# Kernel tuning notes

Measured on AMD Instinct MI355X. Metric: run time of the kernel, lower is better.

## Reference

```python
import jax, jax.numpy as jnp
import numpy as np

# Static multi-scale pyramid (H, W per level); Nv = sum(H*W) = 13294
SPATIAL = np.array([[100, 100], [50, 50], [25, 25], [13, 13]], dtype=np.int64)
B, C, NH, NL, NP = 2, 256, 8, 4, 4
D = C // NH
TOT = NH * NL * NP


def setup_inputs() -> dict:
    key = jax.random.key(0)
    ks = jax.random.split(key, 10)
    Nv = int((SPATIAL[:, 0] * SPATIAL[:, 1]).sum())
    Nq = Nv
    query = jax.random.normal(ks[0], (B, Nq, C), dtype=jnp.float32)
    value = jax.random.normal(ks[1], (B, Nv, C), dtype=jnp.float32)
    reference_points = jax.random.uniform(ks[2], (B, Nq, NL, 2), minval=0.05, maxval=0.95, dtype=jnp.float32)
    spatial_shapes = jnp.asarray(SPATIAL)
    level_start_index = jnp.asarray(np.concatenate([[0], np.cumsum(SPATIAL[:, 0] * SPATIAL[:, 1])[:-1]]))
    # sampling_offsets: small random weight + the rotated-grid bias from _reset_parameters
    W_off = 0.01 * jax.random.normal(ks[3], (C, TOT * 2), dtype=jnp.float32)
    thetas = np.arange(NH, dtype=np.float64) * (2.0 * np.pi / NH)
    grid = np.stack([np.cos(thetas), np.sin(thetas)], -1)
    grid = grid / np.abs(grid).max(-1, keepdims=True)
    grid = np.tile(grid[:, None, None, :], (1, NL, NP, 1)) * (np.arange(NP) + 1)[None, None, :, None]
    b_off = jnp.asarray(grid.reshape(-1), dtype=jnp.float32)
    W_attn = 0.01 * jax.random.normal(ks[4], (C, TOT), dtype=jnp.float32)
    b_attn = jnp.zeros((TOT,), jnp.float32)
    W_val = jax.random.normal(ks[5], (C, C), dtype=jnp.float32) / np.sqrt(C)
    b_val = jnp.zeros((C,), jnp.float32)
    W_out = jax.random.normal(ks[6], (C, C), dtype=jnp.float32) / np.sqrt(C)
    b_out = jnp.zeros((C,), jnp.float32)
    return {"query": query, "value": value, "reference_points": reference_points,
            "spatial_shapes": spatial_shapes, "level_start_index": level_start_index,
            "W_off": W_off, "b_off": b_off, "W_attn": W_attn, "b_attn": b_attn,
            "W_val": W_val, "b_val": b_val, "W_out": W_out, "b_out": b_out}


def _bilinear(vl, loc, H, W):
    # vl: [B, h, H*W, D]; loc: [B, Nq, h, P, 2] normalized (x, y) in [0,1]
    # Matches F.grid_sample(mode='bilinear', padding_mode='zeros', align_corners=False)
    Bb, h, _, Dd = vl.shape
    Nq, P = loc.shape[1], loc.shape[3]
    x = loc[..., 0] * W - 0.5
    y = loc[..., 1] * H - 0.5
    x0 = jnp.floor(x)
    y0 = jnp.floor(y)
    fx = x - x0
    fy = y - y0
    out = jnp.zeros((Bb, h, Nq * P, Dd), vl.dtype)
    corners = ((0, 0, (1 - fx) * (1 - fy)), (1, 0, fx * (1 - fy)),
               (0, 1, (1 - fx) * fy), (1, 1, fx * fy))
    for dx, dy, w in corners:
        xi = x0 + dx
        yi = y0 + dy
        valid = (xi >= 0) & (xi < W) & (yi >= 0) & (yi < H)
        idx = (jnp.clip(yi, 0, H - 1) * W + jnp.clip(xi, 0, W - 1)).astype(jnp.int32)
        idx = idx.transpose(0, 2, 1, 3).reshape(Bb, h, Nq * P)          # [B,h,Nq*P]
        wv = (w * valid).transpose(0, 2, 1, 3).reshape(Bb, h, Nq * P)   # [B,h,Nq*P]
        g = jnp.take_along_axis(vl, idx[..., None], axis=2)             # [B,h,Nq*P,D]
        out = out + g * wv[..., None]
    return out.reshape(Bb, h, Nq, P, Dd)


def reference(query, value, reference_points, spatial_shapes, level_start_index,
              W_off, b_off, W_attn, b_attn, W_val, b_val, W_out, b_out):
    Bb, Nq, Cc = query.shape
    v = (value @ W_val + b_val).reshape(Bb, -1, NH, D)                  # [B,Nv,h,D]
    off = (query @ W_off + b_off).reshape(Bb, Nq, NH, NL, NP, 2)
    attn = jax.nn.softmax((query @ W_attn + b_attn).reshape(Bb, Nq, NH, NL * NP), axis=-1)
    attn = attn.reshape(Bb, Nq, NH, NL, NP)
    # offset normalizer is (W, H) per level
    norm = jnp.asarray(SPATIAL[:, ::-1].copy(), dtype=query.dtype)      # [L,2]
    loc = reference_points[:, :, None, :, None, :] + off / norm[None, None, None, :, None, :]
    starts = np.concatenate([[0], np.cumsum(SPATIAL[:, 0] * SPATIAL[:, 1])])
    out_acc = jnp.zeros((Bb, NH, Nq, D), query.dtype)
    for l in range(NL):
        H, W = int(SPATIAL[l, 0]), int(SPATIAL[l, 1])
        vl = v[:, int(starts[l]):int(starts[l + 1])].transpose(0, 2, 1, 3)  # [B,h,HW,D]
        samp = _bilinear(vl, loc[:, :, :, l], H, W)                     # [B,h,Nq,P,D]
        w_l = attn[:, :, :, l].transpose(0, 2, 1, 3)                    # [B,h,Nq,P]
        out_acc = out_acc + jnp.einsum('bhqpd,bhqp->bhqd', samp, w_l)
    out = out_acc.transpose(0, 2, 1, 3).reshape(Bb, Nq, Cc)
    return out @ W_out + b_out
```

## Files before the change

### kernel.cpp

```cpp
#include <hip/hip_runtime.h>
#include <hip/hip_bf16.h>

#define NQ  13294
#define NV  13294
#define BQ  26588

typedef __attribute__((ext_vector_type(8))) short short8;
typedef __attribute__((ext_vector_type(4))) float f32x4;

static __device__ __forceinline__ ushort f2bf(float f) {
    unsigned int x = __float_as_uint(f);
    unsigned int r = (x + 0x7fffu + ((x >> 16) & 1u)) >> 16;
    return (ushort)r;
}
static __device__ __forceinline__ uint cvtpk_bf16(float a, float b) {
    uint r;
    asm("v_cvt_pk_bf16_f32 %0, %1, %2" : "=v"(r) : "v"(a), "v"(b));
    return r;
}
static __device__ __forceinline__ uint cvtpk_f16(float a, float b) {
    uint r;
    asm("v_cvt_pkrtz_f16_f32 %0, %1, %2" : "=v"(r) : "v"(a), "v"(b));
    return r;
}
static __device__ __forceinline__ float f16lo(uint u) {
    _Float16 h; ushort t = (ushort)(u & 0xffffu);
    __builtin_memcpy(&h, &t, 2); return (float)h;
}
static __device__ __forceinline__ float f16hi(uint u) {
    _Float16 h; ushort t = (ushort)(u >> 16);
    __builtin_memcpy(&h, &t, 2); return (float)h;
}

__global__ __launch_bounds__(256) void prep_weights(
    const float* __restrict__ Wv, const float* __restrict__ Wo,
    const float* __restrict__ Wa, const float* __restrict__ Wu,
    const float* __restrict__ bo, const float* __restrict__ ba,
    ushort* __restrict__ tWv, ushort* __restrict__ tWoa,
    ushort* __restrict__ tWu, float* __restrict__ boa) {
    int i = blockIdx.x * 256 + threadIdx.x;
    if (i < 65536) {
        int n = i >> 8, k = i & 255;
        tWv[i] = f2bf(Wv[k * 256 + n]);
    } else if (i < 65536 + 98304) {
        int j = i - 65536;
        int n = j >> 8, k = j & 255;
        tWoa[j] = f2bf(n < 256 ? Wo[k * 256 + n] : Wa[k * 128 + (n - 256)]);
    } else if (i < 229376) {
        int j = i - 163840;
        int n = j >> 8, k = j & 255;
        tWu[j] = f2bf(Wu[k * 256 + n]);
    } else if (i < 229760) {
        int j = i - 229376;
        boa[j] = j < 256 ? bo[j] : ba[j - 256];
    }
}

#define LDP 40

template<int AF32>
static __device__ __forceinline__ void gemm_core(
    const void* __restrict__ Aptr, const ushort* __restrict__ Bt,
    const float* __restrict__ bias, void* __restrict__ Cout,
    int M, int N, int out_mode, int mblk, int nblk,
    ushort* sA, ushort* sB) {
    const int tid = threadIdx.x;
    const int wid = tid >> 6;
    const int lane = tid & 63;
    const int row0 = mblk * 128;
    const int col0 = nblk * 128;
    const int wr = (wid >> 1) * 64;
    const int wc = (wid & 1) * 64;

    f32x4 acc[4][4];
#pragma unroll
    for (int m = 0; m < 4; ++m)
#pragma unroll
        for (int n = 0; n < 4; ++n) acc[m][n] = (f32x4){0.f, 0.f, 0.f, 0.f};

    for (int kk = 0; kk < 256; kk += 32) {
        __syncthreads();
#pragma unroll
        for (int it = 0; it < 2; ++it) {
            int chunk = tid + it * 256;
            int r = chunk >> 2;
            int seg = chunk & 3;
            int gr = row0 + r; gr = gr < M ? gr : M - 1;
            uint4 wa;
            if (AF32) {
                const float* Af = (const float*)Aptr + (size_t)gr * 256 + kk + seg * 8;
                float4 f0 = *reinterpret_cast<const float4*>(Af);
                float4 f1 = *reinterpret_cast<const float4*>(Af + 4);
                wa.x = cvtpk_bf16(f0.x, f0.y);
                wa.y = cvtpk_bf16(f0.z, f0.w);
                wa.z = cvtpk_bf16(f1.x, f1.y);
                wa.w = cvtpk_bf16(f1.z, f1.w);
            } else {
                wa = *reinterpret_cast<const uint4*>((const ushort*)Aptr + (size_t)gr * 256 + kk + seg * 8);
            }
            *reinterpret_cast<uint4*>(&sA[r * LDP + seg * 8]) = wa;
            int gc = col0 + r;
            uint4 vb4 = *reinterpret_cast<const uint4*>(Bt + (size_t)gc * 256 + kk + seg * 8);
            *reinterpret_cast<uint4*>(&sB[r * LDP + seg * 8]) = vb4;
        }
        __syncthreads();

        short8 a[4], b[4];
#pragma unroll
        for (int m = 0; m < 4; ++m)
            a[m] = *reinterpret_cast<const short8*>(&sA[(wr + m * 16 + (lane & 15)) * LDP + (lane >> 4) * 8]);
#pragma unroll
        for (int n = 0; n < 4; ++n)
            b[n] = *reinterpret_cast<const short8*>(&sB[(wc + n * 16 + (lane & 15)) * LDP + (lane >> 4) * 8]);
#pragma unroll
        for (int m = 0; m < 4; ++m)
#pragma unroll
            for (int n = 0; n < 4; ++n)
                acc[m][n] = __builtin_amdgcn_mfma_f32_16x16x32_bf16(a[m], b[n], acc[m][n], 0, 0, 0);
    }

    const int lr = (lane >> 4) * 4;
    const int lc = lane & 15;
#pragma unroll
    for (int m = 0; m < 4; ++m) {
#pragma unroll
        for (int n = 0; n < 4; ++n) {
            int gcol = col0 + wc + n * 16 + lc;
            float bv = bias[gcol];
#pragma unroll
            for (int j = 0; j < 4; ++j) {
                int grow = row0 + wr + m * 16 + lr + j;
                if (grow < M) {
                    float vv = acc[m][n][j] + bv;
                    if (out_mode == 0) {
                        ((float*)Cout)[(size_t)grow * N + gcol] = vv;
                    } else if (out_mode == 2) {
                        ((ushort*)Cout)[(size_t)grow * N + gcol] = (ushort)(cvtpk_f16(vv, vv) & 0xffffu);
                    } else {
                        int bb = grow >= NV;
                        int pix = grow - bb * NV;
                        int h = gcol >> 5, ch = gcol & 31;
                        ((ushort*)Cout)[(((size_t)(bb * 8 + h)) * NV + pix) * 32 + ch] = f2bf(vv);
                    }
                }
            }
        }
    }
}

__global__ __launch_bounds__(256) void gemm_fused(
    const float* __restrict__ value, const float* __restrict__ query,
    const ushort* __restrict__ tWv, const ushort* __restrict__ tWoa,
    const float* __restrict__ bval, const float* __restrict__ boa,
    ushort* __restrict__ vproj_t, ushort* __restrict__ offattn) {
    __shared__ ushort sA[128 * LDP];
    __shared__ ushort sB[128 * LDP];
    const bool g1 = blockIdx.y < 2;
    gemm_core<1>(g1 ? (const void*)value : (const void*)query,
                 g1 ? tWv : tWoa, g1 ? bval : boa,
                 g1 ? (void*)vproj_t : (void*)offattn,
                 BQ, g1 ? 256 : 384, g1 ? 3 : 2,
                 blockIdx.x, g1 ? blockIdx.y : blockIdx.y - 2, sA, sB);
}

__global__ __launch_bounds__(256) void gemm_out(
    const ushort* __restrict__ outacc, const ushort* __restrict__ tWu,
    const float* __restrict__ bout, float* __restrict__ dout) {
    __shared__ ushort sA[128 * LDP];
    __shared__ ushort sB[128 * LDP];
    gemm_core<0>(outacc, tWu, bout, dout, BQ, 256, 0, blockIdx.x, blockIdx.y, sA, sB);
}

__global__ __launch_bounds__(256) void msda_sample(
    const ushort* __restrict__ offattn,
    const float* __restrict__ refp,
    const ushort* __restrict__ vt,
    ushort* __restrict__ out_acc) {
    __shared__ int4 s_tbl[4][128];

    const int tid = threadIdx.x;
    const int qi = tid >> 6;
    const int lane = tid & 63;
    const int bq = blockIdx.x * 4 + qi;
    const int b = bq / NQ;
    const int q = bq - b * NQ;
    const int h = lane >> 3;

    const ushort* oa = offattn + (size_t)bq * 384;
    const int t0 = lane * 2;
    uint lgu = *reinterpret_cast<const uint*>(oa + 256 + t0);
    float lg0 = f16lo(lgu), lg1 = f16hi(lgu);
    float m = fmaxf(lg0, lg1);
    m = fmaxf(m, __shfl_xor(m, 1));
    m = fmaxf(m, __shfl_xor(m, 2));
    m = fmaxf(m, __shfl_xor(m, 4));
    float e0 = __expf(lg0 - m), e1 = __expf(lg1 - m);
    float ssum = e0 + e1;
    ssum += __shfl_xor(ssum, 1);
    ssum += __shfl_xor(ssum, 2);
    ssum += __shfl_xor(ssum, 4);
    float inv = 1.f / ssum;

    uint2 offu = *reinterpret_cast<const uint2*>(oa + 2 * t0);
    const int l = (t0 >> 2) & 3;
    const int   Wi = (l == 0) ? 100 : (l == 1) ? 50 : (l == 2) ? 25 : 13;
    const float Wf = (float)Wi;
    float rx = refp[(((size_t)b * NQ + q) * 4 + l) * 2 + 0];
    float ry = refp[(((size_t)b * NQ + q) * 4 + l) * 2 + 1];

#pragma unroll
    for (int j = 0; j < 2; ++j) {
        float e = (j ? e1 : e0) * inv;
        float ox = j ? f16lo(offu.y) : f16lo(offu.x);
        float oy = j ? f16hi(offu.y) : f16hi(offu.x);
        float x = fmaf(rx, Wf, ox) - 0.5f;
        float y = fmaf(ry, Wf, oy) - 0.5f;
        float x0f = floorf(x), y0f = floorf(y);
        float fx = x - x0f, fy = y - y0f;
        int x0 = (int)x0f, y0 = (int)y0f;
        float wa = (x0 >= 0 && x0 < Wi)         ? e * (1.f - fx) : 0.f;
        float wb = (x0 + 1 >= 0 && x0 + 1 < Wi) ? e * fx         : 0.f;
        float wy0 = (y0 >= 0 && y0 < Wi)         ? (1.f - fy) : 0.f;
        float wy1 = (y0 + 1 >= 0 && y0 + 1 < Wi) ? fy         : 0.f;
        int s = 2 * (lane & 7) + j;
        int4 ent;
        ent.x = (x0 & 0xffff) | (y0 << 16);
        ent.y = (int)cvtpk_f16(wa, wb);
        ent.z = (int)cvtpk_f16(wy0, wy1);
        ent.w = 0;
        s_tbl[qi][h * 16 + (s ^ h)] = ent;
    }
    __syncthreads();

    const int xbit = (lane >> 2) & 1;
    const int cg = lane & 3;
    const ushort* vh = vt + ((size_t)(b * 8 + h) * NV) * 32 + cg * 8;
    float acc[8] = {0.f, 0.f, 0.f, 0.f, 0.f, 0.f, 0.f, 0.f};

#pragma unroll
    for (int ss = 0; ss < 16; ++ss) {
        const int l2 = ss >> 2;
        const int Wi2 = (l2 == 0) ? 100 : (l2 == 1) ? 50 : (l2 == 2) ? 25 : 13;
        const int st2 = (l2 == 0) ? 0 : (l2 == 1) ? 10000 : (l2 == 2) ? 12500 : 13125;
        int4 ent = s_tbl[qi][h * 16 + (ss ^ h)];
        int x0 = (int)(short)(ent.x & 0xffff);
        int y0 = ent.x >> 16;
        float wx = xbit ? f16hi((uint)ent.y) : f16lo((uint)ent.y);
        float wy0 = f16lo((uint)ent.z), wy1 = f16hi((uint)ent.z);
        int px  = min(max(x0 + xbit, 0), Wi2 - 1);
        int py0 = min(max(y0, 0), Wi2 - 1);
        int py1 = min(max(y0 + 1, 0), Wi2 - 1);
        size_t p0 = (size_t)(st2 + py0 * Wi2 + px) * 32;
        size_t p1 = (size_t)(st2 + py1 * Wi2 + px) * 32;
        uint4 g0 = *reinterpret_cast<const uint4*>(vh + p0);
        uint4 g1 = *reinterpret_cast<const uint4*>(vh + p1);
        float w0 = wx * wy0, w1 = wx * wy1;
        acc[0] = fmaf(__uint_as_float(g0.x << 16), w0, acc[0]);
        acc[1] = fmaf(__uint_as_float(g0.x & 0xffff0000u), w0, acc[1]);
        acc[2] = fmaf(__uint_as_float(g0.y << 16), w0, acc[2]);
        acc[3] = fmaf(__uint_as_float(g0.y & 0xffff0000u), w0, acc[3]);
        acc[4] = fmaf(__uint_as_float(g0.z << 16), w0, acc[4]);
        acc[5] = fmaf(__uint_as_float(g0.z & 0xffff0000u), w0, acc[5]);
        acc[6] = fmaf(__uint_as_float(g0.w << 16), w0, acc[6]);
        acc[7] = fmaf(__uint_as_float(g0.w & 0xffff0000u), w0, acc[7]);
        acc[0] = fmaf(__uint_as_float(g1.x << 16), w1, acc[0]);
        acc[1] = fmaf(__uint_as_float(g1.x & 0xffff0000u), w1, acc[1]);
        acc[2] = fmaf(__uint_as_float(g1.y << 16), w1, acc[2]);
        acc[3] = fmaf(__uint_as_float(g1.y & 0xffff0000u), w1, acc[3]);
        acc[4] = fmaf(__uint_as_float(g1.z << 16), w1, acc[4]);
        acc[5] = fmaf(__uint_as_float(g1.z & 0xffff0000u), w1, acc[5]);
        acc[6] = fmaf(__uint_as_float(g1.w << 16), w1, acc[6]);
        acc[7] = fmaf(__uint_as_float(g1.w & 0xffff0000u), w1, acc[7]);
    }

#pragma unroll
    for (int i = 0; i < 8; ++i) acc[i] += __shfl_xor(acc[i], 4);
    if (xbit == 0) {
        uint4 o;
        o.x = cvtpk_bf16(acc[0], acc[1]);
        o.y = cvtpk_bf16(acc[2], acc[3]);
        o.z = cvtpk_bf16(acc[4], acc[5]);
        o.w = cvtpk_bf16(acc[6], acc[7]);
        *reinterpret_cast<uint4*>(out_acc + (size_t)bq * 256 + h * 32 + cg * 8) = o;
    }
}

extern "C" void kernel_launch(void* const* d_in, const int* in_sizes, int n_in,
                              void* d_out, int out_size, void* d_ws, size_t ws_size,
                              hipStream_t stream) {
    const float* query  = (const float*)d_in[0];
    const float* value  = (const float*)d_in[1];
    const float* refp   = (const float*)d_in[2];
    const float* W_off  = (const float*)d_in[5];
    const float* b_off  = (const float*)d_in[6];
    const float* W_attn = (const float*)d_in[7];
    const float* b_attn = (const float*)d_in[8];
    const float* W_val  = (const float*)d_in[9];
    const float* b_val  = (const float*)d_in[10];
    const float* W_out  = (const float*)d_in[11];
    const float* b_out  = (const float*)d_in[12];

    const size_t ROWB = (size_t)BQ * 256 * 2;
    char* ws = (char*)d_ws;
    ushort* vproj_t = (ushort*)(ws);
    ushort* outacc  = (ushort*)(ws + ROWB);
    ushort* offattn = (ushort*)(ws + 2 * ROWB);
    char*   wbase   = ws + 2 * ROWB + (size_t)BQ * 384 * 2;
    ushort* tWv  = (ushort*)(wbase);
    ushort* tWoa = tWv + 65536;
    ushort* tWu  = tWoa + 98304;
    float*  boa  = (float*)(tWu + 65536);

    prep_weights<<<(229760 + 255) / 256, 256, 0, stream>>>(
        W_val, W_off, W_attn, W_out, b_off, b_attn, tWv, tWoa, tWu, boa);

    gemm_fused<<<dim3(208, 5), 256, 0, stream>>>(
        value, query, tWv, tWoa, b_val, boa, vproj_t, offattn);

    msda_sample<<<BQ / 4, 256, 0, stream>>>(offattn, refp, vproj_t, outacc);

    gemm_out<<<dim3(208, 2), 256, 0, stream>>>(outacc, tWu, b_out, (float*)d_out);
}
```

Baseline: 107.9 us.

## Store projected values as fp16, use fma_mix in sampler, tile weight transpose

The value projection is now written as fp16 instead of bf16. The sampler accumulates with v_fma_mix_f32, which reads the fp16 halves directly and drops the shift and mask unpacking. The sampling table now holds precomputed clamped row offsets and packed column offsets, which removes the clamp and address math from the inner loop. The weight-prep kernel is rewritten as 64x64 tiled transposes through shared memory for coalesced reads. Risks are fp16 range and precision on the values and one extra LDS read per sample.

```diff
diff --git a/kernel.cpp b/kernel.cpp
--- a/kernel.cpp
+++ b/kernel.cpp
@@ -30,6 +30,14 @@
 static __device__ __forceinline__ float f16hi(uint u) {
     _Float16 h; ushort t = (ushort)(u >> 16);
     __builtin_memcpy(&h, &t, 2); return (float)h;
+}
+static __device__ __forceinline__ float fmamix_lo(float acc, uint g, float w) {
+    asm("v_fma_mix_f32 %0, %1, %2, %0 op_sel_hi:[1,0,0]" : "+v"(acc) : "v"(g), "v"(w));
+    return acc;
+}
+static __device__ __forceinline__ float fmamix_hi(float acc, uint g, float w) {
+    asm("v_fma_mix_f32 %0, %1, %2, %0 op_sel:[1,0,0] op_sel_hi:[1,0,0]" : "+v"(acc) : "v"(g), "v"(w));
+    return acc;
 }
 
 __global__ __launch_bounds__(256) void prep_weights(
@@ -38,21 +46,30 @@
     const float* __restrict__ bo, const float* __restrict__ ba,
     ushort* __restrict__ tWv, ushort* __restrict__ tWoa,
     ushort* __restrict__ tWu, float* __restrict__ boa) {
-    int i = blockIdx.x * 256 + threadIdx.x;
-    if (i < 65536) {
-        int n = i >> 8, k = i & 255;
-        tWv[i] = f2bf(Wv[k * 256 + n]);
-    } else if (i < 65536 + 98304) {
-        int j = i - 65536;
-        int n = j >> 8, k = j & 255;
-        tWoa[j] = f2bf(n < 256 ? Wo[k * 256 + n] : Wa[k * 128 + (n - 256)]);
-    } else if (i < 229376) {
-        int j = i - 163840;
-        int n = j >> 8, k = j & 255;
-        tWu[j] = f2bf(Wu[k * 256 + n]);
-    } else if (i < 229760) {
-        int j = i - 229376;
-        boa[j] = j < 256 ? bo[j] : ba[j - 256];
+    const int blk = blockIdx.x;
+    const int tid = threadIdx.x;
+    if (blk == 56) {
+        if (tid < 256) boa[tid] = bo[tid];
+        int j = tid + 256;
+        if (j < 384) boa[j] = ba[j - 256];
+        return;
+    }
+    __shared__ float t[64][65];
+    const float* src; ushort* dst; int srcN, k0, n0, drow0;
+    if (blk < 16)      { int u = blk;      src = Wv; srcN = 256; dst = tWv;  k0 = (u >> 2) * 64; n0 = (u & 3) * 64; drow0 = n0; }
+    else if (blk < 32) { int u = blk - 16; src = Wo; srcN = 256; dst = tWoa; k0 = (u >> 2) * 64; n0 = (u & 3) * 64; drow0 = n0; }
+    else if (blk < 40) { int u = blk - 32; src = Wa; srcN = 128; dst = tWoa; k0 = (u >> 1) * 64; n0 = (u & 1) * 64; drow0 = 256 + n0; }
+    else               { int u = blk - 40; src = Wu; srcN = 256; dst = tWu;  k0 = (u >> 2) * 64; n0 = (u & 3) * 64; drow0 = n0; }
+#pragma unroll
+    for (int it = 0; it < 16; ++it) {
+        int idx = tid + it * 256, r = idx >> 6, c = idx & 63;
+        t[r][c] = src[(size_t)(k0 + r) * srcN + n0 + c];
+    }
+    __syncthreads();
+#pragma unroll
+    for (int it = 0; it < 16; ++it) {
+        int idx = tid + it * 256, r = idx >> 6, c = idx & 63;
+        dst[(size_t)(drow0 + r) * 256 + k0 + c] = f2bf(t[c][r]);
     }
 }
 
@@ -140,7 +157,8 @@
                         int bb = grow >= NV;
                         int pix = grow - bb * NV;
                         int h = gcol >> 5, ch = gcol & 31;
-                        ((ushort*)Cout)[(((size_t)(bb * 8 + h)) * NV + pix) * 32 + ch] = f2bf(vv);
+                        ((ushort*)Cout)[(((size_t)(bb * 8 + h)) * NV + pix) * 32 + ch] =
+                            (ushort)(cvtpk_f16(vv, vv) & 0xffffu);
                     }
                 }
             }
@@ -177,6 +195,7 @@
     const ushort* __restrict__ vt,
     ushort* __restrict__ out_acc) {
     __shared__ int4 s_tbl[4][128];
+    __shared__ uint s_wy[4][128];
 
     const int tid = threadIdx.x;
     const int qi = tid >> 6;
@@ -204,6 +223,7 @@
     uint2 offu = *reinterpret_cast<const uint2*>(oa + 2 * t0);
     const int l = (t0 >> 2) & 3;
     const int   Wi = (l == 0) ? 100 : (l == 1) ? 50 : (l == 2) ? 25 : 13;
+    const int   st = (l == 0) ? 0 : (l == 1) ? 10000 : (l == 2) ? 12500 : 13125;
     const float Wf = (float)Wi;
     float rx = refp[(((size_t)b * NQ + q) * 4 + l) * 2 + 0];
     float ry = refp[(((size_t)b * NQ + q) * 4 + l) * 2 + 1];
@@ -218,59 +238,46 @@
         float x0f = floorf(x), y0f = floorf(y);
         float fx = x - x0f, fy = y - y0f;
         int x0 = (int)x0f, y0 = (int)y0f;
-        float wa = (x0 >= 0 && x0 < Wi)         ? e * (1.f - fx) : 0.f;
-        float wb = (x0 + 1 >= 0 && x0 + 1 < Wi) ? e * fx         : 0.f;
+        float wx0 = (x0 >= 0 && x0 < Wi)         ? e * (1.f - fx) : 0.f;
+        float wx1 = (x0 + 1 >= 0 && x0 + 1 < Wi) ? e * fx         : 0.f;
         float wy0 = (y0 >= 0 && y0 < Wi)         ? (1.f - fy) : 0.f;
         float wy1 = (y0 + 1 >= 0 && y0 + 1 < Wi) ? fy         : 0.f;
+        int px0 = min(max(x0, 0), Wi - 1) * 64;
+        int px1 = min(max(x0 + 1, 0), Wi - 1) * 64;
+        int py0 = min(max(y0, 0), Wi - 1);
+        int py1 = min(max(y0 + 1, 0), Wi - 1);
         int s = 2 * (lane & 7) + j;
-        int4 ent;
-        ent.x = (x0 & 0xffff) | (y0 << 16);
-        ent.y = (int)cvtpk_f16(wa, wb);
-        ent.z = (int)cvtpk_f16(wy0, wy1);
-        ent.w = 0;
-        s_tbl[qi][h * 16 + (s ^ h)] = ent;
+        int ei = h * 16 + (s ^ h);
+        s_tbl[qi][ei] = make_int4((st + py0 * Wi) * 64, (st + py1 * Wi) * 64,
+                                  px0 | (px1 << 16), (int)cvtpk_f16(wx0, wx1));
+        s_wy[qi][ei] = cvtpk_f16(wy0, wy1);
     }
     __syncthreads();
 
     const int xbit = (lane >> 2) & 1;
     const int cg = lane & 3;
-    const ushort* vh = vt + ((size_t)(b * 8 + h) * NV) * 32 + cg * 8;
+    const char* vh = (const char*)vt + ((size_t)(b * 8 + h) * NV) * 64 + cg * 16;
     float acc[8] = {0.f, 0.f, 0.f, 0.f, 0.f, 0.f, 0.f, 0.f};
 
 #pragma unroll
     for (int ss = 0; ss < 16; ++ss) {
-        const int l2 = ss >> 2;
-        const int Wi2 = (l2 == 0) ? 100 : (l2 == 1) ? 50 : (l2 == 2) ? 25 : 13;
-        const int st2 = (l2 == 0) ? 0 : (l2 == 1) ? 10000 : (l2 == 2) ? 12500 : 13125;
-        int4 ent = s_tbl[qi][h * 16 + (ss ^ h)];
-        int x0 = (int)(short)(ent.x & 0xffff);
-        int y0 = ent.x >> 16;
-        float wx = xbit ? f16hi((uint)ent.y) : f16lo((uint)ent.y);
-        float wy0 = f16lo((uint)ent.z), wy1 = f16hi((uint)ent.z);
-        int px  = min(max(x0 + xbit, 0), Wi2 - 1);
-        int py0 = min(max(y0, 0), Wi2 - 1);
-        int py1 = min(max(y0 + 1, 0), Wi2 - 1);
-        size_t p0 = (size_t)(st2 + py0 * Wi2 + px) * 32;
-        size_t p1 = (size_t)(st2 + py1 * Wi2 + px) * 32;
-        uint4 g0 = *reinterpret_cast<const uint4*>(vh + p0);
-        uint4 g1 = *reinterpret_cast<const uint4*>(vh + p1);
-        float w0 = wx * wy0, w1 = wx * wy1;
-        acc[0] = fmaf(__uint_as_float(g0.x << 16), w0, acc[0]);
-        acc[1] = fmaf(__uint_as_float(g0.x & 0xffff0000u), w0, acc[1]);
-        acc[2] = fmaf(__uint_as_float(g0.y << 16), w0, acc[2]);
-        acc[3] = fmaf(__uint_as_float(g0.y & 0xffff0000u), w0, acc[3]);
-        acc[4] = fmaf(__uint_as_float(g0.z << 16), w0, acc[4]);
-        acc[5] = fmaf(__uint_as_float(g0.z & 0xffff0000u), w0, acc[5]);
-        acc[6] = fmaf(__uint_as_float(g0.w << 16), w0, acc[6]);
-        acc[7] = fmaf(__uint_as_float(g0.w & 0xffff0000u), w0, acc[7]);
-        acc[0] = fmaf(__uint_as_float(g1.x << 16), w1, acc[0]);
-        acc[1] = fmaf(__uint_as_float(g1.x & 0xffff0000u), w1, acc[1]);
-        acc[2] = fmaf(__uint_as_float(g1.y << 16), w1, acc[2]);
-        acc[3] = fmaf(__uint_as_float(g1.y & 0xffff0000u), w1, acc[3]);
-        acc[4] = fmaf(__uint_as_float(g1.z << 16), w1, acc[4]);
-        acc[5] = fmaf(__uint_as_float(g1.z & 0xffff0000u), w1, acc[5]);
-        acc[6] = fmaf(__uint_as_float(g1.w << 16), w1, acc[6]);
-        acc[7] = fmaf(__uint_as_float(g1.w & 0xffff0000u), w1, acc[7]);
+        int ei = h * 16 + (ss ^ h);
+        int4 ent = s_tbl[qi][ei];
+        uint wyp = s_wy[qi][ei];
+        int pxo = xbit ? (ent.z >> 16) : (ent.z & 0xffff);
+        float wx = xbit ? f16hi((uint)ent.w) : f16lo((uint)ent.w);
+        float w0 = wx * f16lo(wyp);
+        float w1 = wx * f16hi(wyp);
+        uint4 g0 = *reinterpret_cast<const uint4*>(vh + (uint)(ent.x + pxo));
+        uint4 g1 = *reinterpret_cast<const uint4*>(vh + (uint)(ent.y + pxo));
+        acc[0] = fmamix_lo(acc[0], g0.x, w0); acc[1] = fmamix_hi(acc[1], g0.x, w0);
+        acc[2] = fmamix_lo(acc[2], g0.y, w0); acc[3] = fmamix_hi(acc[3], g0.y, w0);
+        acc[4] = fmamix_lo(acc[4], g0.z, w0); acc[5] = fmamix_hi(acc[5], g0.z, w0);
+        acc[6] = fmamix_lo(acc[6], g0.w, w0); acc[7] = fmamix_hi(acc[7], g0.w, w0);
+        acc[0] = fmamix_lo(acc[0], g1.x, w1); acc[1] = fmamix_hi(acc[1], g1.x, w1);
+        acc[2] = fmamix_lo(acc[2], g1.y, w1); acc[3] = fmamix_hi(acc[3], g1.y, w1);
+        acc[4] = fmamix_lo(acc[4], g1.z, w1); acc[5] = fmamix_hi(acc[5], g1.z, w1);
+        acc[6] = fmamix_lo(acc[6], g1.w, w1); acc[7] = fmamix_hi(acc[7], g1.w, w1);
     }
 
 #pragma unroll
@@ -311,7 +318,7 @@
     ushort* tWu  = tWoa + 98304;
     float*  boa  = (float*)(tWu + 65536);
 
-    prep_weights<<<(229760 + 255) / 256, 256, 0, stream>>>(
+    prep_weights<<<57, 256, 0, stream>>>(
         W_val, W_off, W_attn, W_out, b_off, b_attn, tWv, tWoa, tWu, boa);
 
     gemm_fused<<<dim3(208, 5), 256, 0, stream>>>(
```

Result: no change. 109.5 us (+1.5%).
